# Performance work log

Hardware: AMD Instinct MI355X
Metric: run time of the kernel (lower is better)

## Reference

```python
import jax, jax.numpy as jnp
import numpy as np

N_NODES = 150000
N_EDGES = 2400000


def setup_inputs() -> dict:
    key = jax.random.key(0)
    ks = jax.random.split(key, 7)
    x = jax.random.normal(ks[0], (N_NODES, 9), dtype=jnp.float32)
    edge_index = jax.random.randint(ks[1], (2, N_EDGES), 0, N_NODES, dtype=jnp.int32)
    edge_weight = jax.random.uniform(ks[2], (N_EDGES,), dtype=jnp.float32, minval=0.1, maxval=1.0)
    W1 = jax.random.normal(ks[3], (9, 32), dtype=jnp.float32) * (1.0 / np.sqrt(9))
    b1 = jnp.zeros((32,), dtype=jnp.float32)
    W2 = jax.random.normal(ks[4], (32, 7), dtype=jnp.float32) * (1.0 / np.sqrt(32))
    b2 = jnp.zeros((7,), dtype=jnp.float32)
    return {"x": x, "edge_index": edge_index, "edge_weight": edge_weight,
            "W1": W1, "b1": b1, "W2": W2, "b2": b2}


def gcn_norm(edge_index, edge_weight, num_nodes):
    # PyG gcn_norm: add self-loops (weight 1), symmetric D^-1/2 A D^-1/2
    row, col = edge_index[0], edge_index[1]
    loop = jnp.arange(num_nodes, dtype=edge_index.dtype)
    row = jnp.concatenate([row, loop])
    col = jnp.concatenate([col, loop])
    w = jnp.concatenate([edge_weight, jnp.ones((num_nodes,), edge_weight.dtype)])
    deg = jax.ops.segment_sum(w, col, num_segments=num_nodes)  # [N]
    dinv = jnp.where(deg > 0, jax.lax.rsqrt(deg), 0.0)
    norm = dinv[row] * w * dinv[col]  # [E+N]
    return row, col, norm


def gcn_conv(x, W, b, row, col, norm, num_nodes):
    h = x @ W                                   # [N, out]
    msg = norm[:, None] * h[row]                # [E+N, out] gather + scale
    out = jax.ops.segment_sum(msg, col, num_segments=num_nodes)  # scatter-add
    return out + b


def reference(x, edge_index, edge_weight, W1, b1, W2, b2):
    n = x.shape[0]
    row, col, norm = gcn_norm(edge_index, edge_weight, n)
    h = jax.nn.relu(gcn_conv(x, W1, b1, row, col, norm, n))
    # dropout is identity in eval mode
    h = gcn_conv(h, W2, b2, row, col, norm, n)
    return jax.nn.log_softmax(h, axis=1)
```

## Files before the change

### kernel.cpp

```cpp
#include <hip/hip_runtime.h>
#include <hip/hip_fp16.h>

constexpr int F_IN  = 9;
constexpr int F_HID = 32;
constexpr int F_OUT = 7;

constexpr int NBKT   = 586;
constexpr int BCAP   = 4864;
constexpr int CHUNK  = 4096;
constexpr int EPT    = CHUNK / 1024;

__device__ __forceinline__ int nt_load_int(const int* p) {
    return __builtin_nontemporal_load(p);
}
__device__ __forceinline__ unsigned pack_h2(float a, float b) {
    return (unsigned)__half_as_ushort(__float2half(a)) |
           ((unsigned)__half_as_ushort(__float2half(b)) << 16);
}
__device__ __forceinline__ float2 unpack_h2(unsigned u) {
    return make_float2(__half2float(__ushort_as_half((unsigned short)(u & 0xffffu))),
                       __half2float(__ushort_as_half((unsigned short)(u >> 16))));
}

__global__ __launch_bounds__(1024) void k_hist(
    const int* __restrict__ col, int* __restrict__ ghist, int E)
{
    __shared__ int h[NBKT];
    const int tid = threadIdx.x;
    for (int i = tid; i < NBKT; i += 1024) h[i] = 0;
    __syncthreads();
    const int t0 = blockIdx.x * CHUNK;
    const int kend = min(CHUNK, E - t0);
    for (int k = tid; k < kend; k += 1024)
        atomicAdd(&h[col[t0 + k] >> 8], 1);
    __syncthreads();
    int* g = ghist + (size_t)blockIdx.x * NBKT;
    for (int i = tid; i < NBKT; i += 1024) g[i] = h[i];
}

__global__ __launch_bounds__(256) void k_scan(
    int* __restrict__ ghist, int* __restrict__ cnt, int nchunk)
{
    __shared__ int sc[256];
    const int b = blockIdx.x, tid = threadIdx.x;
    const int per = (nchunk + 255) / 256;
    const int i0 = tid * per, i1 = min(i0 + per, nchunk);

    int sum = 0;
    for (int i = i0; i < i1; ++i) sum += ghist[(size_t)i * NBKT + b];
    sc[tid] = sum; __syncthreads();
    for (int d = 1; d < 256; d <<= 1) {
        int u = (tid >= d) ? sc[tid - d] : 0;
        __syncthreads();
        sc[tid] += u; __syncthreads();
    }
    int run = sc[tid] - sum;
    for (int i = i0; i < i1; ++i) {
        int v = ghist[(size_t)i * NBKT + b];
        ghist[(size_t)i * NBKT + b] = run;
        run += v;
    }
    if (tid == 255) cnt[b] = run;
}

__global__ __launch_bounds__(1024) void k_scat(
    const int* __restrict__ row, const int* __restrict__ col,
    const float* __restrict__ w, const int* __restrict__ ghist,
    int* __restrict__ irA, unsigned char* __restrict__ irB, int E)
{
    __shared__ int           sRW[CHUNK];
    __shared__ int           sDst[CHUNK];
    __shared__ unsigned char sCL[CHUNK];
    __shared__ int hist[NBKT];
    __shared__ int lcur[NBKT];
    __shared__ int sbase[NBKT];
    __shared__ int sc[1024];

    const int tid = threadIdx.x;
    const int* g = ghist + (size_t)blockIdx.x * NBKT;
    for (int i = tid; i < NBKT; i += 1024) { sbase[i] = g[i]; hist[i] = 0; lcur[i] = 0; }
    __syncthreads();

    const int t0 = blockIdx.x * CHUNK;
    const int kend = min(CHUNK, E - t0);

    int rRW[EPT], rBC[EPT], nr = 0;
    for (int k = tid; k < kend; k += 1024) {
        int e = t0 + k;
        int c = col[e];
        int wq = min((int)(w[e] * 16384.0f + 0.5f), 16383);
        rRW[nr] = (row[e] << 14) | wq;
        rBC[nr] = c;
        atomicAdd(&hist[c >> 8], 1);
        ++nr;
    }
    __syncthreads();

    int v = (tid < NBKT) ? hist[tid] : 0;
    sc[tid] = v; __syncthreads();
    for (int d = 1; d < 1024; d <<= 1) {
        int u = (tid >= d) ? sc[tid - d] : 0;
        __syncthreads();
        sc[tid] += u; __syncthreads();
    }
    if (tid < NBKT) hist[tid] = sc[tid] - v;
    __syncthreads();

    for (int q = 0; q < nr; ++q) {
        int c = rBC[q];
        int b = c >> 8;
        int rank = atomicAdd(&lcur[b], 1);
        int p = hist[b] + rank;
        sRW[p] = rRW[q];
        sCL[p] = (unsigned char)(c & 255);
        int gp = sbase[b] + rank;
        sDst[p] = (gp < BCAP) ? (b * BCAP + gp) : -1;
    }
    __syncthreads();

    for (int p = tid; p < kend; p += 1024) {
        int d = sDst[p];
        if (d >= 0) { irA[d] = sRW[p]; irB[d] = sCL[p]; }
    }
}

__global__ __launch_bounds__(1024) void k_sortbucket(
    const int* __restrict__ irA, const unsigned char* __restrict__ irB,
    int* __restrict__ csr4, const int* __restrict__ cnt,
    const float* __restrict__ x, int4* __restrict__ meta,
    unsigned* __restrict__ xdh, int N)
{
    __shared__ int           srw[BCAP];
    __shared__ unsigned char scb[BCAP];
    __shared__ int   hist[256];
    __shared__ float wsum[256];
    __shared__ int   nbase[256];
    __shared__ int   scur[256];

    const int b    = blockIdx.x;
    const int tid  = threadIdx.x;
    const int base = b * BCAP;
    const int c_n  = min(cnt[b], BCAP);

    if (tid < 256) { hist[tid] = 0; wsum[tid] = 0.0f; scur[tid] = 0; }
    __syncthreads();

    for (int k = tid; k < c_n; k += 1024) {
        int rw = irA[base + k];
        unsigned char c = irB[base + k];
        srw[k] = rw;
        scb[k] = c;
        atomicAdd(&hist[c], 1);
        atomicAdd(&wsum[c], (float)(rw & 16383) * (1.0f / 16384.0f));
    }
    __syncthreads();

    int v = 0;
    if (tid < 256) { v = hist[tid]; nbase[tid] = v; }
    __syncthreads();
    for (int d = 1; d < 256; d <<= 1) {
        int u = (tid >= d && tid < 256) ? nbase[tid - d] : 0;
        __syncthreads();
        if (tid < 256) nbase[tid] += u;
        __syncthreads();
    }
    if (tid < 256) {
        int excl = nbase[tid] - v;
        __syncthreads();
        nbase[tid] = excl;
    } else {
        __syncthreads();
    }

    if (tid < 256) {
        int node = b * 256 + tid;
        if (node < N) {
            float dv = rsqrtf(1.0f + wsum[tid]);
            meta[node] = make_int4(base + nbase[tid], v, __float_as_int(dv), 0);
            float xv[F_IN];
            #pragma unroll
            for (int j = 0; j < F_IN; ++j) xv[j] = dv * x[(size_t)node * F_IN + j];
            size_t o = (size_t)node * 6;
            xdh[o + 0] = pack_h2(xv[0], xv[1]);
            xdh[o + 1] = pack_h2(xv[2], xv[3]);
            xdh[o + 2] = pack_h2(xv[4], xv[5]);
            xdh[o + 3] = pack_h2(xv[6], xv[7]);
            xdh[o + 4] = pack_h2(xv[8], 0.0f);
            xdh[o + 5] = 0u;
        }
    }
    __syncthreads();

    for (int k = tid; k < c_n; k += 1024) {
        int rw = srw[k];
        unsigned char c = scb[k];
        int r = atomicAdd(&scur[c], 1);
        csr4[base + nbase[c] + r] = rw;
    }
}

__global__ __launch_bounds__(256) void k_g1mlp(
    const int* __restrict__ csr4, const int4* __restrict__ meta,
    const unsigned* __restrict__ xdh,
    const float* __restrict__ W1, const float* __restrict__ b1,
    const float* __restrict__ W2, unsigned* __restrict__ h2dh, int N)
{
    __shared__ float sW1[F_IN * F_HID];
    __shared__ float sb1[F_HID];
    __shared__ float sW2[F_HID * F_OUT];
    for (int t = threadIdx.x; t < F_IN * F_HID; t += 256) sW1[t] = W1[t];
    for (int t = threadIdx.x; t < F_HID;        t += 256) sb1[t] = b1[t];
    for (int t = threadIdx.x; t < F_HID * F_OUT; t += 256) sW2[t] = W2[t];
    __syncthreads();

    int t   = blockIdx.x * 256 + threadIdx.x;
    int i   = t >> 2;
    int sub = t & 3;
    if (i >= N) return;
    int4 m = meta[i];
    float dv = __int_as_float(m.z);

    float acc[F_IN];
    #pragma unroll
    for (int j = 0; j < F_IN; ++j) acc[j] = 0.0f;
    if (sub == 0) {
        size_t o = (size_t)i * 6;
        uint2 u01 = *reinterpret_cast<const uint2*>(xdh + o);
        uint2 u23 = *reinterpret_cast<const uint2*>(xdh + o + 2);
        unsigned u4 = xdh[o + 4];
        float2 f0 = unpack_h2(u01.x), f1 = unpack_h2(u01.y),
               f2 = unpack_h2(u23.x), f3 = unpack_h2(u23.y),
               f4 = unpack_h2(u4);
        acc[0] = f0.x; acc[1] = f0.y; acc[2] = f1.x; acc[3] = f1.y;
        acc[4] = f2.x; acc[5] = f2.y; acc[6] = f3.x; acc[7] = f3.y;
        acc[8] = f4.x;
    }
    int s = m.x, tend = m.x + m.y;
    for (int e = s + sub; e < tend; e += 4) {
        int v = nt_load_int(&csr4[e]);
        int r = (int)((unsigned)v >> 14);
        float wv = (float)(v & 16383) * (1.0f / 16384.0f);
        size_t o = (size_t)r * 6;
        uint2 u01 = *reinterpret_cast<const uint2*>(xdh + o);
        uint2 u23 = *reinterpret_cast<const uint2*>(xdh + o + 2);
        unsigned u4 = xdh[o + 4];
        float2 f0 = unpack_h2(u01.x), f1 = unpack_h2(u01.y),
               f2 = unpack_h2(u23.x), f3 = unpack_h2(u23.y),
               f4 = unpack_h2(u4);
        acc[0] = fmaf(wv, f0.x, acc[0]); acc[1] = fmaf(wv, f0.y, acc[1]);
        acc[2] = fmaf(wv, f1.x, acc[2]); acc[3] = fmaf(wv, f1.y, acc[3]);
        acc[4] = fmaf(wv, f2.x, acc[4]); acc[5] = fmaf(wv, f2.y, acc[5]);
        acc[6] = fmaf(wv, f3.x, acc[6]); acc[7] = fmaf(wv, f3.y, acc[7]);
        acc[8] = fmaf(wv, f4.x, acc[8]);
    }
    #pragma unroll
    for (int d = 1; d < 4; d <<= 1) {
        #pragma unroll
        for (int j = 0; j < F_IN; ++j)
            acc[j] += __shfl_xor(acc[j], d, 4);
    }
    #pragma unroll
    for (int j = 0; j < F_IN; ++j) acc[j] *= dv;

    float o7[F_OUT];
    #pragma unroll
    for (int c = 0; c < F_OUT; ++c) o7[c] = 0.0f;
    int ks = sub * 8;
    #pragma unroll
    for (int k = 0; k < 8; ++k) {
        float hk = sb1[ks + k];
        #pragma unroll
        for (int j = 0; j < F_IN; ++j) hk = fmaf(acc[j], sW1[j * F_HID + ks + k], hk);
        hk = fmaxf(hk, 0.0f);
        #pragma unroll
        for (int c = 0; c < F_OUT; ++c) o7[c] = fmaf(hk, sW2[(ks + k) * F_OUT + c], o7[c]);
    }
    #pragma unroll
    for (int d = 1; d < 4; d <<= 1) {
        #pragma unroll
        for (int c = 0; c < F_OUT; ++c)
            o7[c] += __shfl_xor(o7[c], d, 4);
    }
    float pa = dv * o7[2 * sub];
    float pb = (2 * sub + 1 < F_OUT) ? dv * o7[2 * sub + 1] : 0.0f;
    h2dh[(size_t)i * 4 + sub] = pack_h2(pa, pb);
}

__global__ __launch_bounds__(256) void k_g2ls(
    const int* __restrict__ csr4, const int4* __restrict__ meta,
    const unsigned* __restrict__ h2dh, const float* __restrict__ b2,
    float* __restrict__ out, int N)
{
    int t   = blockIdx.x * 256 + threadIdx.x;
    int i   = t >> 2;
    int sub = t & 3;
    if (i >= N) return;
    int4 m = meta[i];
    float dv = __int_as_float(m.z);

    float acc[F_OUT];
    #pragma unroll
    for (int c = 0; c < F_OUT; ++c) acc[c] = 0.0f;
    if (sub == 0) {
        uint4 h4 = *reinterpret_cast<const uint4*>(h2dh + (size_t)i * 4);
        float2 f0 = unpack_h2(h4.x), f1 = unpack_h2(h4.y),
               f2 = unpack_h2(h4.z), f3 = unpack_h2(h4.w);
        acc[0] = f0.x; acc[1] = f0.y; acc[2] = f1.x; acc[3] = f1.y;
        acc[4] = f2.x; acc[5] = f2.y; acc[6] = f3.x;
    }
    int s = m.x, tend = m.x + m.y;
    for (int e = s + sub; e < tend; e += 4) {
        int v = nt_load_int(&csr4[e]);
        int r = (int)((unsigned)v >> 14);
        float wv = (float)(v & 16383) * (1.0f / 16384.0f);
        uint4 h4 = *reinterpret_cast<const uint4*>(h2dh + (size_t)r * 4);
        float2 f0 = unpack_h2(h4.x), f1 = unpack_h2(h4.y),
               f2 = unpack_h2(h4.z), f3 = unpack_h2(h4.w);
        acc[0] = fmaf(wv, f0.x, acc[0]); acc[1] = fmaf(wv, f0.y, acc[1]);
        acc[2] = fmaf(wv, f1.x, acc[2]); acc[3] = fmaf(wv, f1.y, acc[3]);
        acc[4] = fmaf(wv, f2.x, acc[4]); acc[5] = fmaf(wv, f2.y, acc[5]);
        acc[6] = fmaf(wv, f3.x, acc[6]);
    }
    #pragma unroll
    for (int d = 1; d < 4; d <<= 1) {
        #pragma unroll
        for (int c = 0; c < F_OUT; ++c)
            acc[c] += __shfl_xor(acc[c], d, 4);
    }

    float vv[F_OUT];
    float mx = -1e30f;
    #pragma unroll
    for (int c = 0; c < F_OUT; ++c) {
        vv[c] = dv * acc[c] + b2[c];
        mx = fmaxf(mx, vv[c]);
    }
    float ss = 0.0f;
    #pragma unroll
    for (int c = 0; c < F_OUT; ++c) ss += __expf(vv[c] - mx);
    float ls = __logf(ss);
    for (int c = sub; c < F_OUT; c += 4)
        out[(size_t)i * F_OUT + c] = vv[c] - mx - ls;
}

extern "C" void kernel_launch(void* const* d_in, const int* in_sizes, int n_in,
                              void* d_out, int out_size, void* d_ws, size_t ws_size,
                              hipStream_t stream) {
    const float* x  = (const float*)d_in[0];
    const int*   ei = (const int*)  d_in[1];
    const float* ew = (const float*)d_in[2];
    const float* W1 = (const float*)d_in[3];
    const float* b1 = (const float*)d_in[4];
    const float* W2 = (const float*)d_in[5];
    const float* b2 = (const float*)d_in[6];
    float* out = (float*)d_out;

    const int N = in_sizes[0] / F_IN;
    const int E = in_sizes[2];
    const int* row = ei;
    const int* col = ei + E;
    const int nchunk = (E + CHUNK - 1) / CHUNK;

    char* p = (char*)d_ws;
    int4*     meta  = (int4*)p;      p += sizeof(int4) * (size_t)N;
    int*      irA   = (int*)p;       p += sizeof(int)  * (size_t)NBKT * BCAP;
    int*      csr4  = (int*)p;       p += sizeof(int)  * (size_t)NBKT * BCAP;
    unsigned* xdh   = (unsigned*)p;  p += sizeof(unsigned) * (size_t)N * 6;
    unsigned* h2dh  = (unsigned*)p;  p += sizeof(unsigned) * (size_t)N * 4;
    int*      ghist = (int*)p;       p += sizeof(int) * (size_t)nchunk * NBKT;
    int*      cnt   = (int*)p;       p += sizeof(int) * NBKT;
    unsigned char* irB = (unsigned char*)p;

    const int gN4 = (4 * N + 255) / 256;

    k_hist      <<<nchunk, 1024, 0, stream>>>(col, ghist, E);
    k_scan      <<<NBKT, 256, 0, stream>>>(ghist, cnt, nchunk);
    k_scat      <<<nchunk, 1024, 0, stream>>>(row, col, ew, ghist, irA, irB, E);
    k_sortbucket<<<NBKT, 1024, 0, stream>>>(irA, irB, csr4, cnt, x, meta, xdh, N);
    k_g1mlp     <<<gN4, 256, 0, stream>>>(csr4, meta, xdh, W1, b1, W2, h2dh, N);
    k_g2ls      <<<gN4, 256, 0, stream>>>(csr4, meta, h2dh, b2, out, N);
}
```

Before: 131.1 us.

## Replace histogram+scan passes with per-bucket global atomic cursors in scatter

Drops the separate histogram and column-scan kernels. The scatter kernel now reserves each chunk's slot range in every bucket with an atomicAdd on a padded global cursor, and a tiny init kernel seeds those cursors. This saves one full read of the column array and two launches. In exchange, edge order within a bucket becomes nondeterministic, and the sortbucket kernel now reads each bucket's count back from its cursor.

```diff
diff --git a/kernel.cpp b/kernel.cpp
--- a/kernel.cpp
+++ b/kernel.cpp
@@ -22,50 +22,14 @@
                        __half2float(__ushort_as_half((unsigned short)(u >> 16))));
 }
 
-__global__ __launch_bounds__(1024) void k_hist(
-    const int* __restrict__ col, int* __restrict__ ghist, int E)
-{
-    __shared__ int h[NBKT];
-    const int tid = threadIdx.x;
-    for (int i = tid; i < NBKT; i += 1024) h[i] = 0;
-    __syncthreads();
-    const int t0 = blockIdx.x * CHUNK;
-    const int kend = min(CHUNK, E - t0);
-    for (int k = tid; k < kend; k += 1024)
-        atomicAdd(&h[col[t0 + k] >> 8], 1);
-    __syncthreads();
-    int* g = ghist + (size_t)blockIdx.x * NBKT;
-    for (int i = tid; i < NBKT; i += 1024) g[i] = h[i];
-}
-
-__global__ __launch_bounds__(256) void k_scan(
-    int* __restrict__ ghist, int* __restrict__ cnt, int nchunk)
-{
-    __shared__ int sc[256];
-    const int b = blockIdx.x, tid = threadIdx.x;
-    const int per = (nchunk + 255) / 256;
-    const int i0 = tid * per, i1 = min(i0 + per, nchunk);
-
-    int sum = 0;
-    for (int i = i0; i < i1; ++i) sum += ghist[(size_t)i * NBKT + b];
-    sc[tid] = sum; __syncthreads();
-    for (int d = 1; d < 256; d <<= 1) {
-        int u = (tid >= d) ? sc[tid - d] : 0;
-        __syncthreads();
-        sc[tid] += u; __syncthreads();
-    }
-    int run = sc[tid] - sum;
-    for (int i = i0; i < i1; ++i) {
-        int v = ghist[(size_t)i * NBKT + b];
-        ghist[(size_t)i * NBKT + b] = run;
-        run += v;
-    }
-    if (tid == 255) cnt[b] = run;
+__global__ void k_init(int* __restrict__ bcur) {
+    int i = threadIdx.x + blockIdx.x * 1024;
+    if (i < NBKT) bcur[i * 16] = i * BCAP;
 }
 
 __global__ __launch_bounds__(1024) void k_scat(
     const int* __restrict__ row, const int* __restrict__ col,
-    const float* __restrict__ w, const int* __restrict__ ghist,
+    const float* __restrict__ w, int* __restrict__ bcur,
     int* __restrict__ irA, unsigned char* __restrict__ irB, int E)
 {
     __shared__ int           sRW[CHUNK];
@@ -77,8 +41,7 @@
     __shared__ int sc[1024];
 
     const int tid = threadIdx.x;
-    const int* g = ghist + (size_t)blockIdx.x * NBKT;
-    for (int i = tid; i < NBKT; i += 1024) { sbase[i] = g[i]; hist[i] = 0; lcur[i] = 0; }
+    for (int i = tid; i < NBKT; i += 1024) { hist[i] = 0; lcur[i] = 0; }
     __syncthreads();
 
     const int t0 = blockIdx.x * CHUNK;
@@ -96,6 +59,10 @@
     }
     __syncthreads();
 
+    if (tid < NBKT) {
+        int c = hist[tid];
+        sbase[tid] = c ? atomicAdd(&bcur[tid * 16], c) : 0;
+    }
     int v = (tid < NBKT) ? hist[tid] : 0;
     sc[tid] = v; __syncthreads();
     for (int d = 1; d < 1024; d <<= 1) {
@@ -114,7 +81,7 @@
         sRW[p] = rRW[q];
         sCL[p] = (unsigned char)(c & 255);
         int gp = sbase[b] + rank;
-        sDst[p] = (gp < BCAP) ? (b * BCAP + gp) : -1;
+        sDst[p] = (gp < (b + 1) * BCAP) ? gp : -1;
     }
     __syncthreads();
 
@@ -126,7 +93,7 @@
 
 __global__ __launch_bounds__(1024) void k_sortbucket(
     const int* __restrict__ irA, const unsigned char* __restrict__ irB,
-    int* __restrict__ csr4, const int* __restrict__ cnt,
+    int* __restrict__ csr4, const int* __restrict__ bcur,
     const float* __restrict__ x, int4* __restrict__ meta,
     unsigned* __restrict__ xdh, int N)
 {
@@ -140,7 +107,7 @@
     const int b    = blockIdx.x;
     const int tid  = threadIdx.x;
     const int base = b * BCAP;
-    const int c_n  = min(cnt[b], BCAP);
+    const int c_n  = min(bcur[b * 16] - base, BCAP);
 
     if (tid < 256) { hist[tid] = 0; wsum[tid] = 0.0f; scur[tid] = 0; }
     __syncthreads();
@@ -367,16 +334,14 @@
     int*      csr4  = (int*)p;       p += sizeof(int)  * (size_t)NBKT * BCAP;
     unsigned* xdh   = (unsigned*)p;  p += sizeof(unsigned) * (size_t)N * 6;
     unsigned* h2dh  = (unsigned*)p;  p += sizeof(unsigned) * (size_t)N * 4;
-    int*      ghist = (int*)p;       p += sizeof(int) * (size_t)nchunk * NBKT;
-    int*      cnt   = (int*)p;       p += sizeof(int) * NBKT;
+    int*      bcur  = (int*)p;       p += sizeof(int) * (size_t)NBKT * 16;
     unsigned char* irB = (unsigned char*)p;
 
     const int gN4 = (4 * N + 255) / 256;
 
-    k_hist      <<<nchunk, 1024, 0, stream>>>(col, ghist, E);
-    k_scan      <<<NBKT, 256, 0, stream>>>(ghist, cnt, nchunk);
-    k_scat      <<<nchunk, 1024, 0, stream>>>(row, col, ew, ghist, irA, irB, E);
-    k_sortbucket<<<NBKT, 1024, 0, stream>>>(irA, irB, csr4, cnt, x, meta, xdh, N);
+    k_init      <<<1, 1024, 0, stream>>>(bcur);
+    k_scat      <<<nchunk, 1024, 0, stream>>>(row, col, ew, bcur, irA, irB, E);
+    k_sortbucket<<<NBKT, 1024, 0, stream>>>(irA, irB, csr4, bcur, x, meta, xdh, N);
     k_g1mlp     <<<gN4, 256, 0, stream>>>(csr4, meta, xdh, W1, b1, W2, h2dh, N);
     k_g2ls      <<<gN4, 256, 0, stream>>>(csr4, meta, h2dh, b2, out, N);
 }
```

New measurement: 136.5 us. 1.04x slower.
